# Kernel tuning notes

Measured on AMD Instinct MI355X. Metric: run time of the kernel, lower is better.

## Reference

```python
import jax, jax.numpy as jnp
import numpy as np
from jax import lax


def _sobel():
    kx = jnp.array([[1., 0., -1.], [2., 0., -2.], [1., 0., -1.]], dtype=jnp.float32) / 4.0
    ky = jnp.array([[1., 2., 1.], [0., 0., 0.], [-1., -2., -1.]], dtype=jnp.float32) / 4.0
    return kx, ky


def _depthwise(x, k2d):
    # x: [B,C,H,W]; k2d: [3,3] -> grouped conv with one filter per channel
    C = x.shape[1]
    k = jnp.tile(k2d[None, None].astype(x.dtype), (C, 1, 1, 1))  # [C,1,3,3]
    return lax.conv_general_dilated(x, k, (1, 1), ((1, 1), (1, 1)),
                                    feature_group_count=C,
                                    dimension_numbers=('NCHW', 'OIHW', 'NCHW'))


def setup_inputs() -> dict:
    key = jax.random.key(0)
    ks = jax.random.split(key, 5)
    B, C, H, W = 8, 256, 160, 160
    hidden = max(8, C // 16)  # 16
    ksize = 7
    x = jax.random.normal(ks[0], (B, C, H, W), dtype=jnp.float32)
    w1 = jax.random.normal(ks[1], (hidden, C), dtype=jnp.float32) * (1.0 / np.sqrt(C))
    w2 = jax.random.normal(ks[2], (C, hidden), dtype=jnp.float32) * (1.0 / np.sqrt(hidden))
    spatial_w = jax.random.normal(ks[3], (1, 4, ksize, ksize), dtype=jnp.float32) * (1.0 / np.sqrt(4 * ksize * ksize))
    spatial_b = jnp.zeros((1,), dtype=jnp.float32)
    alpha = jnp.zeros((), dtype=jnp.float32)
    beta = jnp.zeros((), dtype=jnp.float32)
    return {"x": x, "w1": w1, "w2": w2, "spatial_w": spatial_w,
            "spatial_b": spatial_b, "alpha": alpha, "beta": beta}


def reference(x, w1, w2, spatial_w, spatial_b, alpha, beta):
    kx, ky = _sobel()
    gx = _depthwise(x, kx)
    gy = _depthwise(x, ky)
    g = jnp.sqrt(gx * gx + gy * gy + 1e-12)            # [B,C,H,W]

    # channel gate: mean edge magnitude per channel -> small MLP -> sigmoid
    c_vec = g.mean(axis=(-1, -2))                       # [B,C]
    h = jax.nn.relu(c_vec @ w1.T)                       # [B,hidden]
    w = jax.nn.sigmoid(h @ w2.T)[:, :, None, None]      # [B,C,1,1]

    # spatial gate: 4-channel descriptor -> 7x7 conv -> sigmoid
    avg_x = x.mean(axis=1, keepdims=True)
    max_x = x.max(axis=1, keepdims=True)
    avg_g = g.mean(axis=1, keepdims=True)
    max_g = g.max(axis=1, keepdims=True)
    s_in = jnp.concatenate([avg_x, max_x, avg_g, max_g], axis=1)  # [B,4,H,W]
    pad = spatial_w.shape[-1] // 2
    s = lax.conv_general_dilated(s_in, spatial_w, (1, 1), ((pad, pad), (pad, pad)),
                                 dimension_numbers=('NCHW', 'OIHW', 'NCHW'))
    s = jax.nn.sigmoid(s + spatial_b[None, :, None, None])        # [B,1,H,W]

    a = jax.nn.softplus(alpha)
    b = jax.nn.softplus(beta)
    return x * (1.0 + a * s) * (1.0 + b * w)
```

## Files before the change

### kernel.cpp

```cpp
#include <hip/hip_runtime.h>
#include <math.h>

#define B 8
#define C 256
#define H 160
#define W 160
#define HW (H*W)
#define HIDDEN 16

#define CCHUNK 32
#define NCHUNK (C/CCHUNK)
#define W4 (W/4)
#define F4B (HW/4)
#define PBB (F4B/256)
#define PBLKS (B*PBB)

__global__ __launch_bounds__(256) void k1_sobel_stats(
    const float* __restrict__ x, float* __restrict__ part_c,
    float* __restrict__ part_s)
{
    const int tid   = threadIdx.x;
    const int blk   = blockIdx.x;
    const int chunk = blk & (NCHUNK-1);
    const int pblk  = blk >> 3;
    const int f     = pblk * 256 + tid;
    const int b     = f / F4B;
    const int r     = f % F4B;
    const int h     = r / W4;
    const int w     = (r % W4) * 4;
    const int hw    = h * W + w;

    const bool up = (h > 0), dn = (h < H-1), lf = (w > 0), rt = (w+4 < W);
    const float upf = up ? 1.f : 0.f, dnf = dn ? 1.f : 0.f;
    const float lff = lf ? 1.f : 0.f, rtf = rt ? 1.f : 0.f;
    const float f_tl = upf*lff, f_tr = upf*rtf;
    const float f_bl = dnf*lff, f_br = dnf*rtf;
    const int ot = up ? -W : 0;
    const int ob = dn ?  W : 0;
    const int ol = lf ? -1 : 0;
    const int orr= rt ?  4 : 3;

    const float* xp = x + (size_t)(b*C + chunk*CCHUNK) * HW + hw;
    float* pc = part_c + ((size_t)blk*4 + (tid >> 6)) * CCHUNK;

    float4 sum_x = {0,0,0,0}, sum_g = {0,0,0,0};
    float4 max_x = {-INFINITY,-INFINITY,-INFINITY,-INFINITY};
    float4 max_g = {-INFINITY,-INFINITY,-INFINITY,-INFINITY};

    #pragma unroll 2
    for (int cc = 0; cc < CCHUNK; ++cc) {
        const float* q = xp + (size_t)cc * HW;
        float4 t4 = *(const float4*)(q + ot);
        float4 m4 = *(const float4*)(q);
        float4 b4 = *(const float4*)(q + ob);
        float tl = q[ot+ol]*f_tl, tr = q[ot+orr]*f_tr;
        float ml = q[ol]  *lff,   mr = q[orr]  *rtf;
        float bl = q[ob+ol]*f_bl, br = q[ob+orr]*f_br;
        t4.x*=upf; t4.y*=upf; t4.z*=upf; t4.w*=upf;
        b4.x*=dnf; b4.y*=dnf; b4.z*=dnf; b4.w*=dnf;

        const float rt_[6] = { tl, t4.x, t4.y, t4.z, t4.w, tr };
        const float rm_[6] = { ml, m4.x, m4.y, m4.z, m4.w, mr };
        const float rb_[6] = { bl, b4.x, b4.y, b4.z, b4.w, br };

        float g4[4];
        #pragma unroll
        for (int i = 0; i < 4; ++i) {
            float gx = 0.25f * ((rt_[i]-rt_[i+2]) + 2.f*(rm_[i]-rm_[i+2]) + (rb_[i]-rb_[i+2]));
            float gy = 0.25f * ((rt_[i]+2.f*rt_[i+1]+rt_[i+2]) - (rb_[i]+2.f*rb_[i+1]+rb_[i+2]));
            g4[i] = sqrtf(gx*gx + gy*gy + 1e-12f);
        }
        sum_x.x += m4.x; sum_x.y += m4.y; sum_x.z += m4.z; sum_x.w += m4.w;
        max_x.x = fmaxf(max_x.x, m4.x); max_x.y = fmaxf(max_x.y, m4.y);
        max_x.z = fmaxf(max_x.z, m4.z); max_x.w = fmaxf(max_x.w, m4.w);
        sum_g.x += g4[0]; sum_g.y += g4[1]; sum_g.z += g4[2]; sum_g.w += g4[3];
        max_g.x = fmaxf(max_g.x, g4[0]); max_g.y = fmaxf(max_g.y, g4[1]);
        max_g.z = fmaxf(max_g.z, g4[2]); max_g.w = fmaxf(max_g.w, g4[3]);

        float gs = (g4[0]+g4[1]) + (g4[2]+g4[3]);
        #pragma unroll
        for (int off = 32; off; off >>= 1) gs += __shfl_xor(gs, off, 64);
        if ((tid & 63) == 0) pc[cc] = gs;
    }

    float* sp = part_s + (size_t)(chunk*B + b) * 4 * HW + hw;
    *(float4*)(sp)        = sum_x;
    *(float4*)(sp +   HW) = max_x;
    *(float4*)(sp + 2*HW) = sum_g;
    *(float4*)(sp + 3*HW) = max_g;
}

__global__ __launch_bounds__(256) void k1b_combine(
    const float* __restrict__ part_s, float* __restrict__ s_in)
{
    const int g    = blockIdx.x * 256 + threadIdx.x;
    const int b    = g / (4*F4B);
    const int rr   = g % (4*F4B);
    const int plane= rr / F4B;
    const int hw   = (rr % F4B) * 4;

    const float* sp0 = part_s + (size_t)b * 4 * HW + plane*HW + hw;
    const size_t cstride = (size_t)B * 4 * HW;

    float4 v = *(const float4*)(sp0);
    if (plane == 0 || plane == 2) {
        #pragma unroll
        for (int c = 1; c < NCHUNK; ++c) {
            float4 u = *(const float4*)(sp0 + c*cstride);
            v.x += u.x; v.y += u.y; v.z += u.z; v.w += u.w;
        }
        v.x *= (1.f/C); v.y *= (1.f/C); v.z *= (1.f/C); v.w *= (1.f/C);
    } else {
        #pragma unroll
        for (int c = 1; c < NCHUNK; ++c) {
            float4 u = *(const float4*)(sp0 + c*cstride);
            v.x = fmaxf(v.x,u.x); v.y = fmaxf(v.y,u.y);
            v.z = fmaxf(v.z,u.z); v.w = fmaxf(v.w,u.w);
        }
    }
    *(float4*)(s_in + (size_t)b * 4 * HW + plane*HW + hw) = v;
}

__global__ __launch_bounds__(256) void k2_mlp(
    const float* __restrict__ part_c, const float* __restrict__ w1,
    const float* __restrict__ w2, const float* __restrict__ beta,
    float* __restrict__ chanfac)
{
    __shared__ float cv[C];
    __shared__ float hb[HIDDEN];
    const int b   = blockIdx.x;
    const int tid = threadIdx.x;
    const int chunk = tid >> 5;
    const int cc    = tid & (CCHUNK-1);

    float acc = 0.f;
    for (int pbb = 0; pbb < PBB; ++pbb) {
        const int blk = (b*PBB + pbb) * NCHUNK + chunk;
        const float* pcb = part_c + (size_t)blk * 4 * CCHUNK + cc;
        acc += (pcb[0] + pcb[CCHUNK]) + (pcb[2*CCHUNK] + pcb[3*CCHUNK]);
    }
    cv[tid] = acc * (1.f/(float)HW);
    __syncthreads();

    if (tid < HIDDEN) {
        float a = 0.f;
        for (int c = 0; c < C; ++c) a += cv[c] * w1[tid*C + c];
        hb[tid] = fmaxf(a, 0.f);
    }
    __syncthreads();

    float bt = beta[0];
    float sb = (bt > 20.f) ? bt : log1pf(expf(bt));
    float a = 0.f;
    #pragma unroll
    for (int j = 0; j < HIDDEN; ++j) a += hb[j] * w2[tid*HIDDEN + j];
    float gate = 1.f / (1.f + expf(-a));
    chanfac[b*C + tid] = 1.f + sb * gate;
}

__global__ __launch_bounds__(256) void k3_spatial(
    const float* __restrict__ s_in, const float* __restrict__ sw,
    const float* __restrict__ sbias, const float* __restrict__ alpha,
    float* __restrict__ sfac)
{
    __shared__ float wgt[4*49];
    const int tid = threadIdx.x;
    if (tid < 196) wgt[tid] = sw[tid];
    __syncthreads();

    const int p  = blockIdx.x * 256 + tid;
    const int b  = p / HW;
    const int hw = p % HW;
    const int h  = hw / W;
    const int w  = hw % W;

    const float* base = s_in + (size_t)b * 4 * HW;
    float acc = 0.f;
    for (int ci = 0; ci < 4; ++ci) {
        const float* pl = base + ci*HW;
        #pragma unroll
        for (int i = 0; i < 7; ++i) {
            int hh = h + i - 3;
            if (hh < 0 || hh >= H) continue;
            const float* row = pl + hh*W;
            const float* wr  = wgt + ci*49 + i*7;
            #pragma unroll
            for (int j = 0; j < 7; ++j) {
                int ww = w + j - 3;
                float v = (ww >= 0 && ww < W) ? row[ww] : 0.f;
                acc = fmaf(wr[j], v, acc);
            }
        }
    }
    float al = alpha[0];
    float sa = (al > 20.f) ? al : log1pf(expf(al));
    float sg = 1.f / (1.f + expf(-(acc + sbias[0])));
    sfac[p] = 1.f + sa * sg;
}

__global__ __launch_bounds__(256) void k4_combine(
    const float4* __restrict__ x4, const float* __restrict__ sfac,
    const float* __restrict__ chanfac, float4* __restrict__ out4)
{
    const int i = blockIdx.x * 256 + threadIdx.x;
    const int e  = i * 4;
    const int bc = e / HW;
    const int hw = e % HW;
    const int b  = bc / C;

    const float cf = chanfac[bc];
    const float4 s = *(const float4*)&sfac[b*HW + hw];
    float4 xv = x4[i];
    float4 o;
    o.x = xv.x * s.x * cf;
    o.y = xv.y * s.y * cf;
    o.z = xv.z * s.z * cf;
    o.w = xv.w * s.w * cf;
    out4[i] = o;
}

extern "C" void kernel_launch(void* const* d_in, const int* in_sizes, int n_in,
                              void* d_out, int out_size, void* d_ws, size_t ws_size,
                              hipStream_t stream) {
    const float* x     = (const float*)d_in[0];
    const float* w1    = (const float*)d_in[1];
    const float* w2    = (const float*)d_in[2];
    const float* sw    = (const float*)d_in[3];
    const float* sbias = (const float*)d_in[4];
    const float* alpha = (const float*)d_in[5];
    const float* beta  = (const float*)d_in[6];
    float* out = (float*)d_out;

    float* ws = (float*)d_ws;
    float* part_c  = ws;
    float* part_s  = part_c + (size_t)PBLKS*NCHUNK*4*CCHUNK;
    float* s_in    = part_s + (size_t)NCHUNK*B*4*HW;
    float* sfac    = s_in   + (size_t)B*4*HW;
    float* chanfac = sfac   + (size_t)B*HW;

    k1_sobel_stats<<<PBLKS*NCHUNK, 256, 0, stream>>>(x, part_c, part_s);
    k1b_combine  <<<(B*4*F4B)/256, 256, 0, stream>>>(part_s, s_in);
    k2_mlp       <<<B,             256, 0, stream>>>(part_c, w1, w2, beta, chanfac);
    k3_spatial   <<<(B*HW)/256,    256, 0, stream>>>(s_in, sw, sbias, alpha, sfac);
    k4_combine   <<<(B*C*HW/4)/256, 256, 0, stream>>>((const float4*)x, sfac, chanfac, (float4*)out);
}
```

Baseline: 478.4 us.

## Merge fold and MLP kernels, batch shuffles, branchless 7x7 conv, 2x combine

```diff
diff --git a/kernel.cpp b/kernel.cpp
--- a/kernel.cpp
+++ b/kernel.cpp
@@ -14,6 +14,7 @@
 #define F4B (HW/4)
 #define PBB (F4B/256)
 #define PBLKS (B*PBB)
+#define FOLDBLKS ((B*4*F4B)/256)
 
 __global__ __launch_bounds__(256) void k1_sobel_stats(
     const float* __restrict__ x, float* __restrict__ part_c,
@@ -41,13 +42,13 @@
     const int orr= rt ?  4 : 3;
 
     const float* xp = x + (size_t)(b*C + chunk*CCHUNK) * HW + hw;
-    float* pc = part_c + ((size_t)blk*4 + (tid >> 6)) * CCHUNK;
-
+
+    float gsum[CCHUNK];
     float4 sum_x = {0,0,0,0}, sum_g = {0,0,0,0};
     float4 max_x = {-INFINITY,-INFINITY,-INFINITY,-INFINITY};
     float4 max_g = {-INFINITY,-INFINITY,-INFINITY,-INFINITY};
 
-    #pragma unroll 2
+    #pragma unroll
     for (int cc = 0; cc < CCHUNK; ++cc) {
         const float* q = xp + (size_t)cc * HW;
         float4 t4 = *(const float4*)(q + ot);
@@ -68,7 +69,7 @@
         for (int i = 0; i < 4; ++i) {
             float gx = 0.25f * ((rt_[i]-rt_[i+2]) + 2.f*(rm_[i]-rm_[i+2]) + (rb_[i]-rb_[i+2]));
             float gy = 0.25f * ((rt_[i]+2.f*rt_[i+1]+rt_[i+2]) - (rb_[i]+2.f*rb_[i+1]+rb_[i+2]));
-            g4[i] = sqrtf(gx*gx + gy*gy + 1e-12f);
+            g4[i] = __builtin_amdgcn_sqrtf(gx*gx + gy*gy + 1e-12f);
         }
         sum_x.x += m4.x; sum_x.y += m4.y; sum_x.z += m4.z; sum_x.w += m4.w;
         max_x.x = fmaxf(max_x.x, m4.x); max_x.y = fmaxf(max_x.y, m4.y);
@@ -77,10 +78,7 @@
         max_g.x = fmaxf(max_g.x, g4[0]); max_g.y = fmaxf(max_g.y, g4[1]);
         max_g.z = fmaxf(max_g.z, g4[2]); max_g.w = fmaxf(max_g.w, g4[3]);
 
-        float gs = (g4[0]+g4[1]) + (g4[2]+g4[3]);
-        #pragma unroll
-        for (int off = 32; off; off >>= 1) gs += __shfl_xor(gs, off, 64);
-        if ((tid & 63) == 0) pc[cc] = gs;
+        gsum[cc] = (g4[0]+g4[1]) + (g4[2]+g4[3]);
     }
 
     float* sp = part_s + (size_t)(chunk*B + b) * 4 * HW + hw;
@@ -88,48 +86,61 @@
     *(float4*)(sp +   HW) = max_x;
     *(float4*)(sp + 2*HW) = sum_g;
     *(float4*)(sp + 3*HW) = max_g;
-}
-
-__global__ __launch_bounds__(256) void k1b_combine(
-    const float* __restrict__ part_s, float* __restrict__ s_in)
-{
-    const int g    = blockIdx.x * 256 + threadIdx.x;
-    const int b    = g / (4*F4B);
-    const int rr   = g % (4*F4B);
-    const int plane= rr / F4B;
-    const int hw   = (rr % F4B) * 4;
-
-    const float* sp0 = part_s + (size_t)b * 4 * HW + plane*HW + hw;
-    const size_t cstride = (size_t)B * 4 * HW;
-
-    float4 v = *(const float4*)(sp0);
-    if (plane == 0 || plane == 2) {
-        #pragma unroll
-        for (int c = 1; c < NCHUNK; ++c) {
-            float4 u = *(const float4*)(sp0 + c*cstride);
-            v.x += u.x; v.y += u.y; v.z += u.z; v.w += u.w;
-        }
-        v.x *= (1.f/C); v.y *= (1.f/C); v.z *= (1.f/C); v.w *= (1.f/C);
-    } else {
-        #pragma unroll
-        for (int c = 1; c < NCHUNK; ++c) {
-            float4 u = *(const float4*)(sp0 + c*cstride);
-            v.x = fmaxf(v.x,u.x); v.y = fmaxf(v.y,u.y);
-            v.z = fmaxf(v.z,u.z); v.w = fmaxf(v.w,u.w);
-        }
-    }
-    *(float4*)(s_in + (size_t)b * 4 * HW + plane*HW + hw) = v;
-}
-
-__global__ __launch_bounds__(256) void k2_mlp(
+
+    #pragma unroll
+    for (int off = 32; off; off >>= 1) {
+        #pragma unroll
+        for (int cc = 0; cc < CCHUNK; ++cc)
+            gsum[cc] += __shfl_xor(gsum[cc], off, 64);
+    }
+    if ((tid & 63) == 0) {
+        float* pcw = part_c + ((size_t)blk*4 + (tid>>6)) * CCHUNK;
+        #pragma unroll
+        for (int cc = 0; cc < CCHUNK; ++cc) pcw[cc] = gsum[cc];
+    }
+}
+
+__global__ __launch_bounds__(256) void k1b_fold_mlp(
+    const float* __restrict__ part_s, float* __restrict__ s_in,
     const float* __restrict__ part_c, const float* __restrict__ w1,
     const float* __restrict__ w2, const float* __restrict__ beta,
     float* __restrict__ chanfac)
 {
     __shared__ float cv[C];
     __shared__ float hb[HIDDEN];
-    const int b   = blockIdx.x;
     const int tid = threadIdx.x;
+
+    if (blockIdx.x < FOLDBLKS) {
+        const int g    = blockIdx.x * 256 + tid;
+        const int b    = g / (4*F4B);
+        const int rr   = g % (4*F4B);
+        const int plane= rr / F4B;
+        const int hw   = (rr % F4B) * 4;
+
+        const float* sp0 = part_s + (size_t)b * 4 * HW + plane*HW + hw;
+        const size_t cstride = (size_t)B * 4 * HW;
+
+        float4 v = *(const float4*)(sp0);
+        if (plane == 0 || plane == 2) {
+            #pragma unroll
+            for (int c = 1; c < NCHUNK; ++c) {
+                float4 u = *(const float4*)(sp0 + c*cstride);
+                v.x += u.x; v.y += u.y; v.z += u.z; v.w += u.w;
+            }
+            v.x *= (1.f/C); v.y *= (1.f/C); v.z *= (1.f/C); v.w *= (1.f/C);
+        } else {
+            #pragma unroll
+            for (int c = 1; c < NCHUNK; ++c) {
+                float4 u = *(const float4*)(sp0 + c*cstride);
+                v.x = fmaxf(v.x,u.x); v.y = fmaxf(v.y,u.y);
+                v.z = fmaxf(v.z,u.z); v.w = fmaxf(v.w,u.w);
+            }
+        }
+        *(float4*)(s_in + (size_t)b * 4 * HW + plane*HW + hw) = v;
+        return;
+    }
+
+    const int b     = blockIdx.x - FOLDBLKS;
     const int chunk = tid >> 5;
     const int cc    = tid & (CCHUNK-1);
 
@@ -174,22 +185,35 @@
     const int h  = hw / W;
     const int w  = hw % W;
 
-    const float* base = s_in + (size_t)b * 4 * HW;
+    int wc[7]; float wm[7];
+    #pragma unroll
+    for (int j = 0; j < 7; ++j) {
+        int ww = w + j - 3;
+        wm[j] = (ww >= 0 && ww < W) ? 1.f : 0.f;
+        wc[j] = min(max(ww, 0), W-1) - w;
+    }
+    int hc[7]; float hm[7];
+    #pragma unroll
+    for (int i = 0; i < 7; ++i) {
+        int hh = h + i - 3;
+        hm[i] = (hh >= 0 && hh < H) ? 1.f : 0.f;
+        hc[i] = min(max(hh, 0), H-1);
+    }
+
+    const float* base = s_in + (size_t)b * 4 * HW + w;
     float acc = 0.f;
+    #pragma unroll
     for (int ci = 0; ci < 4; ++ci) {
         const float* pl = base + ci*HW;
         #pragma unroll
         for (int i = 0; i < 7; ++i) {
-            int hh = h + i - 3;
-            if (hh < 0 || hh >= H) continue;
-            const float* row = pl + hh*W;
+            const float* row = pl + hc[i]*W;
             const float* wr  = wgt + ci*49 + i*7;
+            float racc = 0.f;
             #pragma unroll
-            for (int j = 0; j < 7; ++j) {
-                int ww = w + j - 3;
-                float v = (ww >= 0 && ww < W) ? row[ww] : 0.f;
-                acc = fmaf(wr[j], v, acc);
-            }
+            for (int j = 0; j < 7; ++j)
+                racc = fmaf(wr[j], row[wc[j]] * wm[j], racc);
+            acc = fmaf(racc, hm[i], acc);
         }
     }
     float al = alpha[0];
@@ -202,21 +226,25 @@
     const float4* __restrict__ x4, const float* __restrict__ sfac,
     const float* __restrict__ chanfac, float4* __restrict__ out4)
 {
-    const int i = blockIdx.x * 256 + threadIdx.x;
-    const int e  = i * 4;
-    const int bc = e / HW;
-    const int hw = e % HW;
-    const int b  = bc / C;
-
-    const float cf = chanfac[bc];
-    const float4 s = *(const float4*)&sfac[b*HW + hw];
-    float4 xv = x4[i];
-    float4 o;
-    o.x = xv.x * s.x * cf;
-    o.y = xv.y * s.y * cf;
-    o.z = xv.z * s.z * cf;
-    o.w = xv.w * s.w * cf;
-    out4[i] = o;
+    const int i0 = blockIdx.x * 512 + threadIdx.x;
+    #pragma unroll
+    for (int k = 0; k < 2; ++k) {
+        const int i  = i0 + k*256;
+        const int e  = i * 4;
+        const int bc = e / HW;
+        const int hw = e % HW;
+        const int b  = bc / C;
+
+        const float cf = chanfac[bc];
+        const float4 s = *(const float4*)&sfac[b*HW + hw];
+        float4 xv = x4[i];
+        float4 o;
+        o.x = xv.x * s.x * cf;
+        o.y = xv.y * s.y * cf;
+        o.z = xv.z * s.z * cf;
+        o.w = xv.w * s.w * cf;
+        out4[i] = o;
+    }
 }
 
 extern "C" void kernel_launch(void* const* d_in, const int* in_sizes, int n_in,
@@ -239,8 +267,7 @@
     float* chanfac = sfac   + (size_t)B*HW;
 
     k1_sobel_stats<<<PBLKS*NCHUNK, 256, 0, stream>>>(x, part_c, part_s);
-    k1b_combine  <<<(B*4*F4B)/256, 256, 0, stream>>>(part_s, s_in);
-    k2_mlp       <<<B,             256, 0, stream>>>(part_c, w1, w2, beta, chanfac);
+    k1b_fold_mlp <<<FOLDBLKS + B,  256, 0, stream>>>(part_s, s_in, part_c, w1, w2, beta, chanfac);
     k3_spatial   <<<(B*HW)/256,    256, 0, stream>>>(s_in, sw, sbias, alpha, sfac);
-    k4_combine   <<<(B*C*HW/4)/256, 256, 0, stream>>>((const float4*)x, sfac, chanfac, (float4*)out);
-}
+    k4_combine   <<<(B*C*HW/4)/512, 256, 0, stream>>>((const float4*)x, sfac, chanfac, (float4*)out);
+}
```

Result: slower. 890.7 us (+86.2%).
